# Kernel optimization log

Measured on AMD Instinct MI355X. Metric: run time of the kernel, lower is better.

Reference implementation:

```python
import jax, jax.numpy as jnp
import numpy as np

MARGIN = 1.0
EPS = 1e-8  # torch.cosine_similarity default eps


def _cosine(a, b):
    num = jnp.sum(a * b, axis=1)
    den = jnp.maximum(jnp.linalg.norm(a, axis=1) * jnp.linalg.norm(b, axis=1), EPS)
    return num / den


def setup_inputs() -> dict:
    key = jax.random.key(0)
    k1, k2 = jax.random.split(key)
    B, D = 8192, 512
    anchor = jax.random.normal(k1, (B, D), dtype=jnp.float32)
    positive = jax.random.normal(k2, (B, D), dtype=jnp.float32)
    return {"anchor": anchor, "positive": positive}


def reference(anchor, positive):
    B = positive.shape[0]
    a_n = anchor / jnp.linalg.norm(anchor, axis=1, keepdims=True)
    p_n = positive / jnp.linalg.norm(positive, axis=1, keepdims=True)
    sim = a_n @ p_n.T                      # [B, B] cosine similarity
    mask = 1.0 - jnp.eye(B, dtype=sim.dtype)
    sim = sim * mask                       # zero diagonal
    # margin branch of NegariveSampler (margin=1): abs(sim - margin), zeros -> -inf, argmax
    score = jnp.abs(sim - MARGIN) * mask
    score = jnp.where(score == 0.0, -jnp.inf, score)
    neg_idx = jnp.argmax(score, axis=1)    # [B]
    neg = p_n[neg_idx]                     # gather normalized positives as negatives
    cos_ap = _cosine(anchor, positive)
    cos_an = _cosine(anchor, neg)
    loss = jax.nn.relu(MARGIN + cos_ap - cos_an)
    return loss.mean()
```

## Files before the change

### kernel.cpp

```cpp
#include <hip/hip_runtime.h>
#include <stdint.h>

typedef int   i32x8  __attribute__((ext_vector_type(8)));
typedef float f32x16 __attribute__((ext_vector_type(16)));

#define B_ROWS 8192
#define D_DIM  512

__device__ __forceinline__ uint32_t enc_f32(float f) {
  uint32_t s = __float_as_uint(f);
  return (s & 0x80000000u) ? ~s : (s | 0x80000000u);
}
__device__ __forceinline__ float dec_f32(uint32_t e) {
  uint32_t s = (e & 0x80000000u) ? (e ^ 0x80000000u) : ~e;
  return __uint_as_float(s);
}


__global__ __launch_bounds__(256) void norm_kernel(
    const float* __restrict__ anchor, const float* __restrict__ positive,
    uint8_t* __restrict__ a8t, uint8_t* __restrict__ p8t,
    float* __restrict__ cos_ap, uint32_t* __restrict__ minenc)
{
  const int wave = threadIdx.x >> 6, lane = threadIdx.x & 63;
  const int r = blockIdx.x * 4 + wave;

  const float4* av = (const float4*)(anchor   + (size_t)r * D_DIM) + lane * 2;
  const float4* pv = (const float4*)(positive + (size_t)r * D_DIM) + lane * 2;
  float4 a0 = av[0], a1 = av[1];
  float4 p0 = pv[0], p1 = pv[1];

  float sa = a0.x*a0.x + a0.y*a0.y + a0.z*a0.z + a0.w*a0.w
           + a1.x*a1.x + a1.y*a1.y + a1.z*a1.z + a1.w*a1.w;
  float sp = p0.x*p0.x + p0.y*p0.y + p0.z*p0.z + p0.w*p0.w
           + p1.x*p1.x + p1.y*p1.y + p1.z*p1.z + p1.w*p1.w;
  float dp = a0.x*p0.x + a0.y*p0.y + a0.z*p0.z + a0.w*p0.w
           + a1.x*p1.x + a1.y*p1.y + a1.z*p1.z + a1.w*p1.w;

#pragma unroll
  for (int d = 1; d < 64; d <<= 1) {
    sa += __shfl_xor(sa, d);
    sp += __shfl_xor(sp, d);
    dp += __shfl_xor(dp, d);
  }

  const float na = sqrtf(sa), np = sqrtf(sp);
  const float ia = 1.0f / na, ip = 1.0f / np;

  float na0 = a0.x*ia, na1 = a0.y*ia, na2 = a0.z*ia, na3 = a0.w*ia;
  float na4 = a1.x*ia, na5 = a1.y*ia, na6 = a1.z*ia, na7 = a1.w*ia;
  float np0 = p0.x*ip, np1 = p0.y*ip, np2 = p0.z*ip, np3 = p0.w*ip;
  float np4 = p1.x*ip, np5 = p1.y*ip, np6 = p1.z*ip, np7 = p1.w*ip;

  uint32_t aw0 = __builtin_amdgcn_cvt_pk_fp8_f32(na0, na1, 0,  false);
  aw0          = __builtin_amdgcn_cvt_pk_fp8_f32(na2, na3, aw0, true);
  uint32_t aw1 = __builtin_amdgcn_cvt_pk_fp8_f32(na4, na5, 0,  false);
  aw1          = __builtin_amdgcn_cvt_pk_fp8_f32(na6, na7, aw1, true);
  uint32_t pw0 = __builtin_amdgcn_cvt_pk_fp8_f32(np0, np1, 0,  false);
  pw0          = __builtin_amdgcn_cvt_pk_fp8_f32(np2, np3, pw0, true);
  uint32_t pw1 = __builtin_amdgcn_cvt_pk_fp8_f32(np4, np5, 0,  false);
  pw1          = __builtin_amdgcn_cvt_pk_fp8_f32(np6, np7, pw1, true);

  const int c = lane & 31;
  const uint32_t A0 = __shfl(aw0, c*2),   A1 = __shfl(aw1, c*2);
  const uint32_t A2 = __shfl(aw0, c*2+1), A3 = __shfl(aw1, c*2+1);
  const uint32_t P0 = __shfl(pw0, c*2),   P1 = __shfl(pw1, c*2);
  const uint32_t P2 = __shfl(pw0, c*2+1), P3 = __shfl(pw1, c*2+1);

  const int kBlk = c >> 2, h = (c >> 1) & 1, j = c & 1;
  const size_t off = ((size_t)((r >> 5) * 8 + kBlk)) * 2048 + j * 1024
                   + ((h * 32 + (r & 31)) * 16);
  if (lane < 32) *(uint4*)(a8t + off) = make_uint4(A0, A1, A2, A3);
  else           *(uint4*)(p8t + off) = make_uint4(P0, P1, P2, P3);

  if (lane == 0) {
    cos_ap[r] = dp / fmaxf(na * np, 1e-8f);
    minenc[r] = 0xFFFFFFFFu;
  }
}

__global__ __launch_bounds__(256, 2) void simmin_kernel(
    const uint8_t* __restrict__ a8t, const uint8_t* __restrict__ p8t,
    uint32_t* __restrict__ minenc)
{
  __shared__ float redmin[4][128];

  const int tid  = threadIdx.x;
  const int lane = tid & 63;
  const int wave = tid >> 6;
  const int half = lane >> 5;
  const int r31  = lane & 31;

  const int bid = blockIdx.x;
  const int blockRow = (bid & 7) * 8 + ((bid >> 3) & 7);
  const int blockCol = bid >> 6;

  f32x16 acc[4][2];
#pragma unroll
  for (int i = 0; i < 4; i++)
#pragma unroll
    for (int j = 0; j < 2; j++)
#pragma unroll
      for (int e = 0; e < 16; e++) acc[i][j][e] = 0.f;

  const uint8_t* aT[4];
#pragma unroll
  for (int mf = 0; mf < 4; mf++)
    aT[mf] = a8t + ((size_t)(blockRow * 4 + mf)) * (8 * 2048) + lane * 16;
  const uint8_t* pT[2];
#pragma unroll
  for (int nf = 0; nf < 2; nf++)
    pT[nf] = p8t + ((size_t)(blockCol * 8 + wave * 2 + nf)) * (8 * 2048) + lane * 16;

  i32x8 af[2][4], bf[2][2];

  auto loadA = [&](int kb, int buf) {
#pragma unroll
    for (int mf = 0; mf < 4; mf++) {
      const uint8_t* t = aT[mf] + kb * 2048;
      const int4 lo = *(const int4*)t;
      const int4 hi = *(const int4*)(t + 1024);
      af[buf][mf] = (i32x8){lo.x, lo.y, lo.z, lo.w, hi.x, hi.y, hi.z, hi.w};
    }
  };
  auto loadB = [&](int kb, int buf) {
#pragma unroll
    for (int nf = 0; nf < 2; nf++) {
      const uint8_t* t = pT[nf] + kb * 2048;
      const int4 lo = *(const int4*)t;
      const int4 hi = *(const int4*)(t + 1024);
      bf[buf][nf] = (i32x8){lo.x, lo.y, lo.z, lo.w, hi.x, hi.y, hi.z, hi.w};
    }
  };

  loadA(0, 0);
  loadB(0, 0);

#pragma unroll
  for (int kb = 0; kb < 8; kb++) {
    const int cur = kb & 1, nxt = cur ^ 1;
    if (kb < 7) { loadA(kb + 1, nxt); loadB(kb + 1, nxt); }

#pragma unroll
    for (int mf = 0; mf < 4; mf++)
#pragma unroll
      for (int nf = 0; nf < 2; nf++)
        acc[mf][nf] = __builtin_amdgcn_mfma_scale_f32_32x32x64_f8f6f4(
            af[cur][mf], bf[cur][nf], acc[mf][nf],
            0, 0,
            0, 0x7F7F7F7F,
            0, 0x7F7F7F7F);
  }

  float rm[4][16];
#pragma unroll
  for (int mf = 0; mf < 4; mf++)
#pragma unroll
    for (int g = 0; g < 16; g++) rm[mf][g] = 3.0e38f;

#pragma unroll
  for (int mf = 0; mf < 4; mf++) {
#pragma unroll
    for (int nf = 0; nf < 2; nf++) {
      const int col = blockCol * 256 + wave * 64 + nf * 32 + r31;
#pragma unroll
      for (int g = 0; g < 16; g++) {
        const int row = blockRow * 128 + mf * 32 + (g & 3) + 8 * (g >> 2) + 4 * half;
        const float v = acc[mf][nf][g];
        rm[mf][g] = (row == col) ? rm[mf][g] : fminf(rm[mf][g], v);
      }
    }
  }
#pragma unroll
  for (int d = 1; d < 32; d <<= 1)
#pragma unroll
    for (int mf = 0; mf < 4; mf++)
#pragma unroll
      for (int g = 0; g < 16; g++)
        rm[mf][g] = fminf(rm[mf][g], __shfl_xor(rm[mf][g], d));

  if (r31 == 0) {
#pragma unroll
    for (int mf = 0; mf < 4; mf++)
#pragma unroll
      for (int g = 0; g < 16; g++)
        redmin[wave][mf * 32 + (g & 3) + 8 * (g >> 2) + 4 * half] = rm[mf][g];
  }
  __syncthreads();

  if (tid < 128) {
    const float m = fminf(fminf(redmin[0][tid], redmin[1][tid]),
                          fminf(redmin[2][tid], redmin[3][tid]));
    atomicMin(&minenc[blockRow * 128 + tid], enc_f32(m));
  }
}

__global__ __launch_bounds__(1024) void finalize_kernel(
    const uint32_t* __restrict__ minenc, const float* __restrict__ cos_ap,
    float* __restrict__ out)
{
  float sum = 0.0f;
#pragma unroll
  for (int r = threadIdx.x; r < B_ROWS; r += 1024)
    sum += fmaxf(0.0f, 1.0f + cos_ap[r] - dec_f32(minenc[r]));

#pragma unroll
  for (int d = 1; d < 64; d <<= 1) sum += __shfl_xor(sum, d);
  __shared__ float s[16];
  if ((threadIdx.x & 63) == 0) s[threadIdx.x >> 6] = sum;
  __syncthreads();
  if (threadIdx.x < 64) {
    float t = (threadIdx.x < 16) ? s[threadIdx.x] : 0.0f;
#pragma unroll
    for (int d = 1; d < 16; d <<= 1) t += __shfl_xor(t, d);
    if (threadIdx.x == 0) out[0] = t * (1.0f / (float)B_ROWS);
  }
}

extern "C" void kernel_launch(void* const* d_in, const int* in_sizes, int n_in,
                              void* d_out, int out_size, void* d_ws, size_t ws_size,
                              hipStream_t stream) {
  const float* anchor   = (const float*)d_in[0];
  const float* positive = (const float*)d_in[1];

  char* ws = (char*)d_ws;
  uint8_t*  a8t    = (uint8_t*)(ws);
  uint8_t*  p8t    = (uint8_t*)(ws + (4ull << 20));
  float*    cos_ap = (float*)(ws + (8ull << 20));
  uint32_t* minenc = (uint32_t*)(ws + (8ull << 20) + (32ull << 10));
  float*    out = (float*)d_out;

  norm_kernel<<<B_ROWS / 4, 256, 0, stream>>>(anchor, positive, a8t, p8t,
                                              cos_ap, minenc);
  simmin_kernel<<<2048, 256, 0, stream>>>(a8t, p8t, minenc);
  finalize_kernel<<<1, 1024, 0, stream>>>(minenc, cos_ap, out);
}
```

Measured before the change: 132.2 us.

## Stage shared A tiles through LDS with direct global-to-LDS loads

Previously all four waves of a block each loaded the same four A fragments from global memory on every k-step. Now each wave copies one quarter of the A tile into a double-buffered LDS array using global_load_lds. All waves then read their A fragments from LDS after a block barrier. This cuts redundant global/L2 traffic for A by a factor of four, at the cost of a __syncthreads per k-step and extra LDS reads.

```diff
diff --git a/kernel.cpp b/kernel.cpp
--- a/kernel.cpp
+++ b/kernel.cpp
@@ -79,10 +79,18 @@
   }
 }
 
+__device__ __forceinline__ void load16_to_lds(const void* g, void* l) {
+  __builtin_amdgcn_global_load_lds(
+      (__attribute__((address_space(1))) uint32_t*)(uintptr_t)(g),
+      (__attribute__((address_space(3))) uint32_t*)(uintptr_t)(l),
+      16, 0, 0);
+}
+
 __global__ __launch_bounds__(256, 2) void simmin_kernel(
     const uint8_t* __restrict__ a8t, const uint8_t* __restrict__ p8t,
     uint32_t* __restrict__ minenc)
 {
+  __shared__ __attribute__((aligned(16))) uint8_t Albuf[2][4 * 2048];
   __shared__ float redmin[4][128];
 
   const int tid  = threadIdx.x;
@@ -103,50 +111,55 @@
 #pragma unroll
       for (int e = 0; e < 16; e++) acc[i][j][e] = 0.f;
 
-  const uint8_t* aT[4];
-#pragma unroll
-  for (int mf = 0; mf < 4; mf++)
-    aT[mf] = a8t + ((size_t)(blockRow * 4 + mf)) * (8 * 2048) + lane * 16;
+  const uint8_t* aStage = a8t + ((size_t)(blockRow * 4 + wave)) * (8 * 2048)
+                        + lane * 16;
+  auto stageA = [&](int kb, int buf) {
+    const uint8_t* src = aStage + (size_t)kb * 2048;
+    load16_to_lds(src,        &Albuf[buf][wave * 2048]);
+    load16_to_lds(src + 1024, &Albuf[buf][wave * 2048 + 1024]);
+  };
+
   const uint8_t* pT[2];
 #pragma unroll
   for (int nf = 0; nf < 2; nf++)
-    pT[nf] = p8t + ((size_t)(blockCol * 8 + wave * 2 + nf)) * (8 * 2048) + lane * 16;
-
-  i32x8 af[2][4], bf[2][2];
-
-  auto loadA = [&](int kb, int buf) {
-#pragma unroll
-    for (int mf = 0; mf < 4; mf++) {
-      const uint8_t* t = aT[mf] + kb * 2048;
-      const int4 lo = *(const int4*)t;
-      const int4 hi = *(const int4*)(t + 1024);
-      af[buf][mf] = (i32x8){lo.x, lo.y, lo.z, lo.w, hi.x, hi.y, hi.z, hi.w};
-    }
-  };
+    pT[nf] = p8t + ((size_t)(blockCol * 8 + wave * 2 + nf)) * (8 * 2048)
+           + lane * 16;
+
+  i32x8 bf[2][2];
   auto loadB = [&](int kb, int buf) {
 #pragma unroll
     for (int nf = 0; nf < 2; nf++) {
-      const uint8_t* t = pT[nf] + kb * 2048;
+      const uint8_t* t = pT[nf] + (size_t)kb * 2048;
       const int4 lo = *(const int4*)t;
       const int4 hi = *(const int4*)(t + 1024);
       bf[buf][nf] = (i32x8){lo.x, lo.y, lo.z, lo.w, hi.x, hi.y, hi.z, hi.w};
     }
   };
 
-  loadA(0, 0);
+  stageA(0, 0);
   loadB(0, 0);
 
 #pragma unroll
   for (int kb = 0; kb < 8; kb++) {
     const int cur = kb & 1, nxt = cur ^ 1;
-    if (kb < 7) { loadA(kb + 1, nxt); loadB(kb + 1, nxt); }
+    __syncthreads();
+
+    i32x8 af[4];
+#pragma unroll
+    for (int mf = 0; mf < 4; mf++) {
+      const int4 lo = *(const int4*)&Albuf[cur][mf * 2048 + lane * 16];
+      const int4 hi = *(const int4*)&Albuf[cur][mf * 2048 + 1024 + lane * 16];
+      af[mf] = (i32x8){lo.x, lo.y, lo.z, lo.w, hi.x, hi.y, hi.z, hi.w};
+    }
+
+    if (kb < 7) { stageA(kb + 1, nxt); loadB(kb + 1, nxt); }
 
 #pragma unroll
     for (int mf = 0; mf < 4; mf++)
 #pragma unroll
       for (int nf = 0; nf < 2; nf++)
         acc[mf][nf] = __builtin_amdgcn_mfma_scale_f32_32x32x64_f8f6f4(
-            af[cur][mf], bf[cur][nf], acc[mf][nf],
+            af[mf], bf[cur][nf], acc[mf][nf],
             0, 0,
             0, 0x7F7F7F7F,
             0, 0x7F7F7F7F);
```

After: 133.3 us. About the same (+0.8%).
